# Optimization experiments

Hardware: AMD Instinct MI355X
Metric: run time of the kernel (lower is better)

The kernel has to match this reference:

```python
import jax, jax.numpy as jnp
import numpy as np
from jax import lax

LRELU = 0.1
SQRT_HALF = 0.7071067811865476
DIM = 128
NUM_PRE = 5          # dilated convs in UpsampleNet
NUM_BLOCKS = 3       # WaveNet blocks
LAYERS_PER_BLOCK = 10
NUM_WN = NUM_BLOCKS * LAYERS_PER_BLOCK  # 30


def conv1d(x, w, b, dilation=1):
    # x: [N,C,L], w: [O,I,K], 'same' padding for odd K
    k = w.shape[-1]
    pad = dilation * (k // 2)
    y = lax.conv_general_dilated(
        x, w, window_strides=(1,), padding=[(pad, pad)],
        rhs_dilation=(dilation,), dimension_numbers=('NCW', 'OIW', 'NCW'))
    return y + b[None, :, None]


def conv_transpose1d(x, w, b, stride=4):
    # kernel 4, stride 4, no padding -> L_out = 4*L
    y = lax.conv_transpose(
        x, w, strides=(stride,), padding='VALID',
        dimension_numbers=('NCW', 'OIW', 'NCW'))
    return y + b[None, :, None]


def setup_inputs() -> dict:
    key = jax.random.key(0)
    ks = iter(jax.random.split(key, 32))
    s = 0.02
    d = {}
    d['mel'] = jax.random.normal(next(ks), (4, 80, 64), jnp.float32)
    d['in_w'] = s * jax.random.normal(next(ks), (DIM, 80, 1), jnp.float32)
    d['in_b'] = jnp.zeros((DIM,), jnp.float32)
    d['pre_ws'] = s * jax.random.normal(next(ks), (NUM_PRE, DIM, DIM, 3), jnp.float32)
    d['pre_bs'] = jnp.zeros((NUM_PRE, DIM), jnp.float32)
    d['up1_w'] = s * jax.random.normal(next(ks), (DIM, DIM, 4), jnp.float32)
    d['up1_b'] = jnp.zeros((DIM,), jnp.float32)
    d['up2_w'] = s * jax.random.normal(next(ks), (DIM, DIM, 4), jnp.float32)
    d['up2_b'] = jnp.zeros((DIM,), jnp.float32)
    d['wn_ws'] = s * jax.random.normal(next(ks), (NUM_WN, 2 * DIM, DIM, 3), jnp.float32)
    d['wn_bs'] = jnp.zeros((NUM_WN, 2 * DIM), jnp.float32)
    d['sk_ws'] = s * jax.random.normal(next(ks), (NUM_WN, DIM, DIM, 1), jnp.float32)
    d['sk_bs'] = jnp.zeros((NUM_WN, DIM), jnp.float32)
    d['out1_w'] = s * jax.random.normal(next(ks), (DIM, DIM, 1), jnp.float32)
    d['out1_b'] = jnp.zeros((DIM,), jnp.float32)
    d['out2_w'] = s * jax.random.normal(next(ks), (DIM, DIM, 1), jnp.float32)
    d['out2_b'] = jnp.zeros((DIM,), jnp.float32)
    d['out3_w'] = s * jax.random.normal(next(ks), (1, DIM, 1), jnp.float32)
    d['out3_b'] = jnp.zeros((1,), jnp.float32)
    return d


def reference(mel, in_w, in_b, pre_ws, pre_bs, up1_w, up1_b, up2_w, up2_b,
              wn_ws, wn_bs, sk_ws, sk_bs,
              out1_w, out1_b, out2_w, out2_b, out3_w, out3_b):
    # ---- UpsampleNet ----
    x = conv1d(mel, in_w, in_b)                       # [N,128,T]
    for i in range(NUM_PRE):
        residual = x
        x = conv1d(x, pre_ws[i], pre_bs[i], dilation=2 ** i)
        x = jax.nn.leaky_relu(x, LRELU)
        x = (x + residual) * SQRT_HALF
    x = jax.nn.leaky_relu(conv_transpose1d(x, up1_w, up1_b), LRELU)
    x = jax.nn.leaky_relu(conv_transpose1d(x, up2_w, up2_b), LRELU)
    N, D, L = x.shape
    x = jnp.broadcast_to(x[:, :, :, None], (N, D, L, 16)).reshape(N, D, L * 16)

    # ---- WaveNet blocks (3 blocks x 10 layers) ----
    skips = jnp.zeros_like(x)
    for li in range(NUM_WN):
        dilation = 2 ** (li % LAYERS_PER_BLOCK)
        residual = x
        g = conv1d(x, wn_ws[li], wn_bs[li], dilation=dilation)  # [N,256,L]
        g_tanh, g_sig = jnp.split(g, 2, axis=1)
        gated = jnp.tanh(g_tanh) * jax.nn.sigmoid(g_sig)
        s = conv1d(gated, sk_ws[li], sk_bs[li])
        skips = skips + s
        x = s + residual

    # ---- Output stack ----
    y = jax.nn.relu(skips)
    y = jax.nn.relu(conv1d(y, out1_w, out1_b))
    y = jax.nn.relu(conv1d(y, out2_w, out2_b))
    y = conv1d(y, out3_w, out3_b)
    return jnp.tanh(y)  # [N,1,L*256]
```

## Files before the change

### kernel.cpp

```cpp
#include <hip/hip_runtime.h>
#include <math.h>

#define LRELU 0.1f
#define SQRT_HALF 0.7071067811865476f

constexpr int T_LEN = 16384;

typedef __attribute__((ext_vector_type(8))) short short8;
typedef __attribute__((ext_vector_type(4))) float f32x4;

union U4S8 { uint4 v; short8 s8; unsigned short us[8]; };

__device__ inline void bsplit(float v, unsigned short& hi, unsigned short& lo) {
    unsigned u = __float_as_uint(v);
    unsigned rh = (u + 0x7FFFu + ((u >> 16) & 1u)) >> 16;
    float fh = __uint_as_float(rh << 16);
    float r = v - fh;
    unsigned u2 = __float_as_uint(r);
    unsigned rl = (u2 + 0x7FFFu + ((u2 >> 16) & 1u)) >> 16;
    hi = (unsigned short)rh; lo = (unsigned short)rl;
}
__device__ inline float b2f(unsigned short s) { return __uint_as_float(((unsigned)s) << 16); }

__device__ inline size_t fidx(int n, int tb, int c, int l) {
    return ((size_t)((n << 10) + tb) * 4 + c) * 64 + l;
}

__device__ inline float fast_gate(float g1, float g2) {
    float ax = fabsf(g1);
    float e = __expf(ax + ax);
    float th = 1.f - 2.f * __builtin_amdgcn_rcpf(e + 1.f);
    th = __uint_as_float(__float_as_uint(th) | (__float_as_uint(g1) & 0x80000000u));
    float sg = __builtin_amdgcn_rcpf(1.f + __expf(-g2));
    return th * sg;
}

__global__ void prep_w3(const float* __restrict__ wn_ws, const float* __restrict__ sk_ws,
                        const float* __restrict__ o1w, const float* __restrict__ o2w,
                        unsigned short* __restrict__ Apk, unsigned short* __restrict__ Spk,
                        unsigned short* __restrict__ Opk1, unsigned short* __restrict__ Opk2)
{
    int b = blockIdx.x, tid = threadIdx.x;
    if (b < 360) {
        __shared__ float sl[256][32];
        int li = b / 12, ks = b % 12;
        int tap = ks >> 2, i0 = (ks & 3) * 32;
        for (int j = tid; j < 8192; j += 256) {
            int o = j >> 5, ii = j & 31;
            sl[o][ii] = wn_ws[((size_t)(li * 256 + o) * 128 + i0 + ii) * 3 + tap];
        }
        __syncthreads();
        size_t obase = ((size_t)(li * 12 + ks)) * 16384;
        for (int e = tid; e < 8192; e += 256) {
            int j = e & 7, l = (e >> 3) & 63, m16 = e >> 9;
            int o = m16 * 16 + (l & 15);
            int ii = 4 * (l >> 4) + (j & 3) + 16 * (j >> 2);
            unsigned short hi, lo; bsplit(sl[o][ii], hi, lo);
            Apk[obase + (size_t)m16 * 1024 + l * 8 + j] = hi;
            Apk[obase + (size_t)m16 * 1024 + 512 + l * 8 + j] = lo;
        }
    } else {
        __shared__ float s2[128][32];
        int bb = b - 360;
        const float* src; unsigned short* dst; int ks2;
        if (bb < 120) { int li = bb / 4; ks2 = bb % 4; src = sk_ws + (size_t)li * 16384; dst = Spk + ((size_t)(li * 4 + ks2)) * 8192; }
        else if (bb < 124) { ks2 = bb - 120; src = o1w; dst = Opk1 + (size_t)ks2 * 8192; }
        else { ks2 = bb - 124; src = o2w; dst = Opk2 + (size_t)ks2 * 8192; }
        int i0 = ks2 * 32;
        for (int j = tid; j < 4096; j += 256) {
            int o = j >> 5, ii = j & 31;
            s2[o][ii] = src[(size_t)o * 128 + i0 + ii];
        }
        __syncthreads();
        for (int e = tid; e < 4096; e += 256) {
            int j = e & 7, l = (e >> 3) & 63, m8 = e >> 9;
            int o = m8 * 16 + (l & 15);
            int ii = 4 * (l >> 4) + (j & 3) + 16 * (j >> 2);
            unsigned short hi, lo; bsplit(s2[o][ii], hi, lo);
            dst[(size_t)m8 * 1024 + l * 8 + j] = hi;
            dst[(size_t)m8 * 1024 + 512 + l * 8 + j] = lo;
        }
    }
}

__global__ void fe_in(const float* __restrict__ mel, const float* __restrict__ w,
                      const float* __restrict__ b, float* __restrict__ out)
{
    __shared__ float mc[80];
    int t = blockIdx.x, n = blockIdx.y, o = threadIdx.x;
    if (o < 80) mc[o] = mel[(n * 80 + o) * 64 + t];
    __syncthreads();
    float acc = b[o];
    #pragma unroll 8
    for (int i = 0; i < 80; i++) acc = fmaf(w[o * 80 + i], mc[i], acc);
    out[((size_t)n * 128 + o) * 64 + t] = acc;
}

__global__ void fe_pre(const float* __restrict__ in, float* __restrict__ out,
                       const float* __restrict__ w, const float* __restrict__ b, int d)
{
    __shared__ float col[3][128];
    int t = blockIdx.x, n = blockIdx.y, o = threadIdx.x;
    #pragma unroll
    for (int s = 0; s < 3; s++) {
        int tt = t + (s - 1) * d;
        col[s][o] = ((unsigned)tt < 64u) ? in[(n * 128 + o) * 64 + tt] : 0.f;
    }
    __syncthreads();
    float acc = b[o];
    const float* wo = w + o * 384;
    #pragma unroll 4
    for (int i = 0; i < 128; i++) {
        acc = fmaf(wo[i * 3 + 0], col[0][i], acc);
        acc = fmaf(wo[i * 3 + 1], col[1][i], acc);
        acc = fmaf(wo[i * 3 + 2], col[2][i], acc);
    }
    float y = acc > 0.f ? acc : LRELU * acc;
    out[(n * 128 + o) * 64 + t] = (y + in[(n * 128 + o) * 64 + t]) * SQRT_HALF;
}

__global__ __launch_bounds__(256, 4)
void fe_up3(const float* __restrict__ in, float* __restrict__ out,
            const float* __restrict__ w, const float* __restrict__ bias, int Lin)
{
    __shared__ float xs[128][16];
    const int n = blockIdx.y, qb = blockIdx.x * 16;
    const int tid = threadIdx.x;
    for (int j = tid; j < 2048; j += 256) {
        int i = j >> 4, qq = j & 15;
        xs[i][qq] = in[(size_t)(n * 128 + i) * Lin + qb + qq];
    }
    __syncthreads();
    const int o = tid & 127, qh = tid >> 7;
    float acc[8][4];
    #pragma unroll
    for (int q = 0; q < 8; q++)
        #pragma unroll
        for (int r = 0; r < 4; r++) acc[q][r] = 0.f;
    const float4* wo = (const float4*)(w + (size_t)o * 512);
    for (int i = 0; i < 128; i++) {
        float4 w4 = wo[i];
        #pragma unroll
        for (int q = 0; q < 8; q++) {
            float xv = xs[i][qh * 8 + q];
            acc[q][0] = fmaf(w4.w, xv, acc[q][0]);
            acc[q][1] = fmaf(w4.z, xv, acc[q][1]);
            acc[q][2] = fmaf(w4.y, xv, acc[q][2]);
            acc[q][3] = fmaf(w4.x, xv, acc[q][3]);
        }
    }
    float bo = bias[o];
    const int Lout = 4 * Lin;
    #pragma unroll
    for (int q = 0; q < 8; q++) {
        float4 v;
        float a0 = acc[q][0] + bo, a1 = acc[q][1] + bo, a2 = acc[q][2] + bo, a3 = acc[q][3] + bo;
        v.x = a0 > 0.f ? a0 : LRELU * a0;
        v.y = a1 > 0.f ? a1 : LRELU * a1;
        v.z = a2 > 0.f ? a2 : LRELU * a2;
        v.w = a3 > 0.f ? a3 : LRELU * a3;
        *(float4*)(out + (size_t)(n * 128 + o) * Lout + (size_t)(qb + qh * 8 + q) * 4) = v;
    }
}

__global__ void fe_repeat_f(const float* __restrict__ x1024,
                            uint4* __restrict__ Xh, uint4* __restrict__ Xl)
{
    __shared__ float sx[128][65];
    const int n = blockIdx.y, tbq = blockIdx.x;
    const int tid = threadIdx.x;
    for (int j = tid; j < 8192; j += 256) {
        int ch = j >> 6, col = j & 63;
        sx[ch][col] = x1024[(size_t)(n * 128 + ch) * 1024 + tbq * 64 + col];
    }
    __syncthreads();
    for (int m = tid; m < 16384; m += 256) {
        int l = m & 63, c = (m >> 6) & 3, tbr = m >> 8;
        U4S8 ho, lo_;
        #pragma unroll
        for (int j = 0; j < 8; j++) {
            int ch = 32 * c + 4 * (l >> 4) + (j & 3) + 16 * (j >> 2);
            unsigned short hi, lo; bsplit(sx[ch][tbr], hi, lo);
            ho.us[j] = hi; lo_.us[j] = lo;
        }
        size_t gi = fidx(n, tbq * 64 + tbr, c, l);
        Xh[gi] = ho.v; Xl[gi] = lo_.v;
    }
}

__global__ __launch_bounds__(256, 4)
void wn_layer(const uint4* __restrict__ Xh, const uint4* __restrict__ Xl,
              uint4* __restrict__ Yh, uint4* __restrict__ Yl,
              const unsigned short* __restrict__ Apk, const float* __restrict__ gb,
              const unsigned short* __restrict__ Spk, const float* __restrict__ skb, int dil)
{
    __shared__ __align__(16) uint4 S[2048];

    const int bxs = ((blockIdx.x & 7) << 5) | (blockIdx.x >> 3);
    const int n = blockIdx.y, tb0 = bxs * 4, t0 = tb0 * 16;
    const int tid = threadIdx.x, lane = tid & 63, wid = tid >> 6;

    f32x4 acc[4][4];
    const f32x4 z4 = {0.f, 0.f, 0.f, 0.f};
    #pragma unroll
    for (int mf = 0; mf < 4; mf++)
        #pragma unroll
        for (int nf = 0; nf < 4; nf++) acc[mf][nf] = z4;

    const short8* ap = (const short8*)Apk;
    const int m16c[4] = {2 * wid, 2 * wid + 1, 8 + 2 * wid, 9 + 2 * wid};

    for (int s = 0; s < 3; s++) {
        const int sh = (s - 1) * dil;
        __syncthreads();
        for (int j = tid; j < 1024; j += 256) {
            int l = j & 63, c = (j >> 6) & 3, nf = j >> 8;
            int t = t0 + nf * 16 + (l & 15) + sh;
            uint4 vh = make_uint4(0u, 0u, 0u, 0u), vl = vh;
            if ((unsigned)t < (unsigned)T_LEN) {
                size_t gi = fidx(n, t >> 4, c, (l & 48) | (t & 15));
                vh = Xh[gi]; vl = Xl[gi];
            }
            S[j] = vh; S[1024 + j] = vl;
        }
        __syncthreads();
        for (int c = 0; c < 4; c++) {
            const int ks = s * 4 + c;
            short8 Ah[4], Al[4];
            #pragma unroll
            for (int mf = 0; mf < 4; mf++) {
                int ib = (ks * 16 + m16c[mf]) * 128 + lane;
                Ah[mf] = ap[ib];
                Al[mf] = ap[ib + 64];
            }
            #pragma unroll
            for (int nf = 0; nf < 4; nf++) {
                U4S8 bh, bl;
                bh.v = S[(nf * 4 + c) * 64 + lane];
                bl.v = S[1024 + (nf * 4 + c) * 64 + lane];
                #pragma unroll
                for (int mf = 0; mf < 4; mf++) {
                    acc[mf][nf] = __builtin_amdgcn_mfma_f32_16x16x32_bf16(Ah[mf], bh.s8, acc[mf][nf], 0, 0, 0);
                    acc[mf][nf] = __builtin_amdgcn_mfma_f32_16x16x32_bf16(Al[mf], bh.s8, acc[mf][nf], 0, 0, 0);
                    acc[mf][nf] = __builtin_amdgcn_mfma_f32_16x16x32_bf16(Ah[mf], bl.s8, acc[mf][nf], 0, 0, 0);
                }
            }
        }
    }
    __syncthreads();

    const int cb = 4 * (lane >> 4);
    float bt[2][4], bsg[2][4];
    #pragma unroll
    for (int mf2 = 0; mf2 < 2; mf2++)
        #pragma unroll
        for (int r = 0; r < 4; r++) {
            int ch = (2 * wid + mf2) * 16 + cb + r;
            bt[mf2][r] = gb[ch];
            bsg[mf2][r] = gb[128 + ch];
        }
    #pragma unroll
    for (int nf = 0; nf < 4; nf++) {
        U4S8 h4, l4;
        #pragma unroll
        for (int mf2 = 0; mf2 < 2; mf2++)
            #pragma unroll
            for (int r = 0; r < 4; r++) {
                float g1 = acc[mf2][nf][r] + bt[mf2][r];
                float g2 = acc[mf2 + 2][nf][r] + bsg[mf2][r];
                float gv = fast_gate(g1, g2);
                unsigned short hi, lo; bsplit(gv, hi, lo);
                h4.us[mf2 * 4 + r] = hi;
                l4.us[mf2 * 4 + r] = lo;
            }
        S[(nf * 4 + wid) * 64 + lane] = h4.v;
        S[1024 + (nf * 4 + wid) * 64 + lane] = l4.v;
    }
    __syncthreads();

    f32x4 acc2[2][4];
    #pragma unroll
    for (int mf2 = 0; mf2 < 2; mf2++)
        #pragma unroll
        for (int nf = 0; nf < 4; nf++) acc2[mf2][nf] = z4;
    const short8* sp = (const short8*)Spk;
    #pragma unroll
    for (int c = 0; c < 4; c++) {
        short8 A2h[2], A2l[2];
        #pragma unroll
        for (int mf2 = 0; mf2 < 2; mf2++) {
            int ib = (c * 8 + 2 * wid + mf2) * 128 + lane;
            A2h[mf2] = sp[ib];
            A2l[mf2] = sp[ib + 64];
        }
        #pragma unroll
        for (int nf = 0; nf < 4; nf++) {
            U4S8 bh, bl;
            bh.v = S[(nf * 4 + c) * 64 + lane];
            bl.v = S[1024 + (nf * 4 + c) * 64 + lane];
            #pragma unroll
            for (int mf2 = 0; mf2 < 2; mf2++) {
                acc2[mf2][nf] = __builtin_amdgcn_mfma_f32_16x16x32_bf16(A2h[mf2], bh.s8, acc2[mf2][nf], 0, 0, 0);
                acc2[mf2][nf] = __builtin_amdgcn_mfma_f32_16x16x32_bf16(A2l[mf2], bh.s8, acc2[mf2][nf], 0, 0, 0);
                acc2[mf2][nf] = __builtin_amdgcn_mfma_f32_16x16x32_bf16(A2h[mf2], bl.s8, acc2[mf2][nf], 0, 0, 0);
            }
        }
    }

    float bo2[2][4];
    #pragma unroll
    for (int mf2 = 0; mf2 < 2; mf2++)
        #pragma unroll
        for (int r = 0; r < 4; r++) bo2[mf2][r] = skb[(2 * wid + mf2) * 16 + cb + r];
    #pragma unroll
    for (int nf = 0; nf < 4; nf++) {
        size_t gi = fidx(n, tb0 + nf, wid, lane);
        U4S8 xh, xl, oh, ol;
        xh.v = Xh[gi]; xl.v = Xl[gi];
        #pragma unroll
        for (int j = 0; j < 8; j++) {
            int mf2 = j >> 2, r = j & 3;
            float xin = b2f(xh.us[j]) + b2f(xl.us[j]);
            float sv = acc2[mf2][nf][r] + bo2[mf2][r];
            unsigned short hi, lo; bsplit(sv + xin, hi, lo);
            oh.us[j] = hi; ol.us[j] = lo;
        }
        Yh[gi] = oh.v; Yl[gi] = ol.v;
    }
}

__global__ __launch_bounds__(256, 2)
void os_fused(const uint4* __restrict__ Fh, const uint4* __restrict__ Fl,
              const uint4* __restrict__ Ih, const uint4* __restrict__ Il,
              const unsigned short* __restrict__ Opk1, const float* __restrict__ o1b,
              const unsigned short* __restrict__ Opk2, const float* __restrict__ o2b,
              const float* __restrict__ o3w, const float* __restrict__ o3b,
              float* __restrict__ out)
{
    __shared__ __align__(16) uint4 SA[2048];
    __shared__ __align__(16) uint4 SB[2048];
    const int n = blockIdx.y, tb0 = blockIdx.x * 4, t0 = tb0 * 16;
    const int tid = threadIdx.x, lane = tid & 63, wid = tid >> 6;
    const int tl = lane & 15, cb = 4 * (lane >> 4);
    const f32x4 z4 = {0.f, 0.f, 0.f, 0.f};
    char* ldsA = (char*)SA;

    for (int j = tid; j < 1024; j += 256) {
        int l = j & 63, c = (j >> 6) & 3, nf = j >> 8;
        size_t gi = fidx(n, tb0 + nf, c, l);
        U4S8 fh, fl, ih, il, ho, lo_;
        fh.v = Fh[gi]; fl.v = Fl[gi]; ih.v = Ih[gi]; il.v = Il[gi];
        #pragma unroll
        for (int e = 0; e < 8; e++) {
            float d = (b2f(fh.us[e]) + b2f(fl.us[e])) - (b2f(ih.us[e]) + b2f(il.us[e]));
            d = fmaxf(d, 0.f);
            unsigned short hi, lo; bsplit(d, hi, lo);
            ho.us[e] = hi; lo_.us[e] = lo;
        }
        SA[j] = ho.v; SA[1024 + j] = lo_.v;
    }
    __syncthreads();

    {
        f32x4 acc[2][4];
        #pragma unroll
        for (int mf2 = 0; mf2 < 2; mf2++)
            #pragma unroll
            for (int nf = 0; nf < 4; nf++) acc[mf2][nf] = z4;
        const short8* op = (const short8*)Opk1;
        #pragma unroll
        for (int c = 0; c < 4; c++) {
            short8 Ah[2], Al[2];
            #pragma unroll
            for (int mf2 = 0; mf2 < 2; mf2++) {
                int ib = (c * 8 + 2 * wid + mf2) * 128 + lane;
                Ah[mf2] = op[ib]; Al[mf2] = op[ib + 64];
            }
            #pragma unroll
            for (int nf = 0; nf < 4; nf++) {
                U4S8 bh, bl;
                bh.v = SA[(nf * 4 + c) * 64 + lane];
                bl.v = SA[1024 + (nf * 4 + c) * 64 + lane];
                #pragma unroll
                for (int mf2 = 0; mf2 < 2; mf2++) {
                    acc[mf2][nf] = __builtin_amdgcn_mfma_f32_16x16x32_bf16(Ah[mf2], bh.s8, acc[mf2][nf], 0, 0, 0);
                    acc[mf2][nf] = __builtin_amdgcn_mfma_f32_16x16x32_bf16(Al[mf2], bh.s8, acc[mf2][nf], 0, 0, 0);
                    acc[mf2][nf] = __builtin_amdgcn_mfma_f32_16x16x32_bf16(Ah[mf2], bl.s8, acc[mf2][nf], 0, 0, 0);
                }
            }
        }
        #pragma unroll
        for (int nf = 0; nf < 4; nf++) {
            U4S8 h4, l4;
            #pragma unroll
            for (int mf2 = 0; mf2 < 2; mf2++)
                #pragma unroll
                for (int r = 0; r < 4; r++) {
                    float v = fmaxf(acc[mf2][nf][r] + o1b[(2 * wid + mf2) * 16 + cb + r], 0.f);
                    unsigned short hi, lo; bsplit(v, hi, lo);
                    h4.us[mf2 * 4 + r] = hi; l4.us[mf2 * 4 + r] = lo;
                }
            SB[(nf * 4 + wid) * 64 + lane] = h4.v;
            SB[1024 + (nf * 4 + wid) * 64 + lane] = l4.v;
        }
    }
    __syncthreads();

    {
        f32x4 acc[2][4];
        #pragma unroll
        for (int mf2 = 0; mf2 < 2; mf2++)
            #pragma unroll
            for (int nf = 0; nf < 4; nf++) acc[mf2][nf] = z4;
        const short8* op = (const short8*)Opk2;
        #pragma unroll
        for (int c = 0; c < 4; c++) {
            short8 Ah[2], Al[2];
            #pragma unroll
            for (int mf2 = 0; mf2 < 2; mf2++) {
                int ib = (c * 8 + 2 * wid + mf2) * 128 + lane;
                Ah[mf2] = op[ib]; Al[mf2] = op[ib + 64];
            }
            #pragma unroll
            for (int nf = 0; nf < 4; nf++) {
                U4S8 bh, bl;
                bh.v = SB[(nf * 4 + c) * 64 + lane];
                bl.v = SB[1024 + (nf * 4 + c) * 64 + lane];
                #pragma unroll
                for (int mf2 = 0; mf2 < 2; mf2++) {
                    acc[mf2][nf] = __builtin_amdgcn_mfma_f32_16x16x32_bf16(Ah[mf2], bh.s8, acc[mf2][nf], 0, 0, 0);
                    acc[mf2][nf] = __builtin_amdgcn_mfma_f32_16x16x32_bf16(Al[mf2], bh.s8, acc[mf2][nf], 0, 0, 0);
                    acc[mf2][nf] = __builtin_amdgcn_mfma_f32_16x16x32_bf16(Ah[mf2], bl.s8, acc[mf2][nf], 0, 0, 0);
                }
            }
        }
        __syncthreads();
        #pragma unroll
        for (int mf2 = 0; mf2 < 2; mf2++) {
            const int ch0 = (2 * wid + mf2) * 16 + cb;
            #pragma unroll
            for (int nf = 0; nf < 4; nf++) {
                int row = nf * 16 + tl, swz = (row & 7) << 4;
                float4 v;
                v.x = fmaxf(acc[mf2][nf][0] + o2b[ch0 + 0], 0.f);
                v.y = fmaxf(acc[mf2][nf][1] + o2b[ch0 + 1], 0.f);
                v.z = fmaxf(acc[mf2][nf][2] + o2b[ch0 + 2], 0.f);
                v.w = fmaxf(acc[mf2][nf][3] + o2b[ch0 + 3], 0.f);
                *(float4*)(ldsA + row * 512 + ((ch0 * 4) ^ swz)) = v;
            }
        }
    }
    __syncthreads();

    {
        const int t_loc = tid >> 2, qq = tid & 3;
        const int row = t_loc, swz = (row & 7) << 4;
        float a = 0.f;
        #pragma unroll
        for (int cc = 0; cc < 8; cc++) {
            int ch = qq * 32 + cc * 4;
            float4 v = *(const float4*)(ldsA + row * 512 + ((ch * 4) ^ swz));
            a += o3w[ch] * v.x + o3w[ch + 1] * v.y + o3w[ch + 2] * v.z + o3w[ch + 3] * v.w;
        }
        a += __shfl_xor(a, 1);
        a += __shfl_xor(a, 2);
        if (qq == 0) out[(size_t)n * T_LEN + t0 + t_loc] = tanhf(a + o3b[0]);
    }
}

extern "C" void kernel_launch(void* const* d_in, const int* in_sizes, int n_in,
                              void* d_out, int out_size, void* d_ws, size_t ws_size,
                              hipStream_t stream)
{
    (void)in_sizes; (void)n_in; (void)out_size; (void)ws_size;
    const float* mel    = (const float*)d_in[0];
    const float* in_w   = (const float*)d_in[1];
    const float* in_b   = (const float*)d_in[2];
    const float* pre_w  = (const float*)d_in[3];
    const float* pre_b  = (const float*)d_in[4];
    const float* up1_w  = (const float*)d_in[5];
    const float* up1_b  = (const float*)d_in[6];
    const float* up2_w  = (const float*)d_in[7];
    const float* up2_b  = (const float*)d_in[8];
    const float* wn_wsp = (const float*)d_in[9];
    const float* wn_bs  = (const float*)d_in[10];
    const float* sk_wsp = (const float*)d_in[11];
    const float* sk_bs  = (const float*)d_in[12];
    const float* o1w = (const float*)d_in[13];
    const float* o1b = (const float*)d_in[14];
    const float* o2w = (const float*)d_in[15];
    const float* o2b = (const float*)d_in[16];
    const float* o3w = (const float*)d_in[17];
    const float* o3b = (const float*)d_in[18];

    char* base = (char*)d_ws;
    uint4* XAh = (uint4*)(base);
    uint4* XAl = (uint4*)(base + 16777216);
    uint4* XBh = (uint4*)(base + 33554432);
    uint4* XBl = (uint4*)(base + 50331648);
    uint4* XCh = (uint4*)(base + 67108864);
    uint4* XCl = (uint4*)(base + 83886080);
    unsigned short* Apk = (unsigned short*)(base + 100663296);
    unsigned short* Spk = (unsigned short*)(base + 112459776);
    unsigned short* Opk1 = (unsigned short*)(base + 114425856);
    unsigned short* Opk2 = (unsigned short*)(base + 114491392);
    float* a64   = (float*)(base + 114556928);
    float* b64   = (float*)(base + 114688000);
    float* x256  = (float*)(base + 114819072);
    float* x1024 = (float*)(base + 115343360);

    prep_w3<<<488, 256, 0, stream>>>(wn_wsp, sk_wsp, o1w, o2w, Apk, Spk, Opk1, Opk2);

    fe_in<<<dim3(64, 4), 128, 0, stream>>>(mel, in_w, in_b, a64);
    fe_pre<<<dim3(64, 4), 128, 0, stream>>>(a64, b64, pre_w + 0 * 49152, pre_b + 0 * 128, 1);
    fe_pre<<<dim3(64, 4), 128, 0, stream>>>(b64, a64, pre_w + 1 * 49152, pre_b + 1 * 128, 2);
    fe_pre<<<dim3(64, 4), 128, 0, stream>>>(a64, b64, pre_w + 2 * 49152, pre_b + 2 * 128, 4);
    fe_pre<<<dim3(64, 4), 128, 0, stream>>>(b64, a64, pre_w + 3 * 49152, pre_b + 3 * 128, 8);
    fe_pre<<<dim3(64, 4), 128, 0, stream>>>(a64, b64, pre_w + 4 * 49152, pre_b + 4 * 128, 16);
    fe_up3<<<dim3(4, 4), 256, 0, stream>>>(b64, x256, up1_w, up1_b, 64);
    fe_up3<<<dim3(16, 4), 256, 0, stream>>>(x256, x1024, up2_w, up2_b, 256);
    fe_repeat_f<<<dim3(16, 4), 256, 0, stream>>>(x1024, XAh, XAl);

    for (int li = 0; li < 30; li++) {
        int d = 1 << (li % 10);
        const uint4 *ih, *il; uint4 *oh, *ol;
        if (li == 0)      { ih = XAh; il = XAl; oh = XBh; ol = XBl; }
        else if (li & 1)  { ih = XBh; il = XBl; oh = XCh; ol = XCl; }
        else              { ih = XCh; il = XCl; oh = XBh; ol = XBl; }
        wn_layer<<<dim3(T_LEN / 64, 4), 256, 0, stream>>>(
            ih, il, oh, ol,
            Apk + (size_t)li * 196608, wn_bs + li * 256,
            Spk + (size_t)li * 32768, sk_bs + li * 128, d);
    }

    os_fused<<<dim3(T_LEN / 64, 4), 256, 0, stream>>>(
        XCh, XCl, XAh, XAl, Opk1, o1b, Opk2, o2b, o3w, o3b, (float*)d_out);
}
```

Measured before the change: 1.887 ms.

## Add direct-global-load WaveNet layer variant for tile-aligned dilations

For dilations that are multiples of 16, the shifted input tiles line up with whole time blocks, so a new kernel variant feeds the MFMAs straight from global memory and skips the shared-memory staging and its barriers. Smaller dilations keep the staged path, which now has its inner channel loop fully unrolled. The shared gate/skip tail is factored into a helper, and the block-index swizzle is removed from both variants. Loading directly from global removes the three staging barriers per layer, but relies on the L2 cache to serve the reuse across warps and may change locality now that the swizzle is gone.

```diff
diff --git a/kernel.cpp b/kernel.cpp
--- a/kernel.cpp
+++ b/kernel.cpp
@@ -188,16 +188,155 @@
     }
 }
 
+__device__ __forceinline__ void wn_tail(
+    f32x4 (&acc)[4][4], uint4* S, const uint4* __restrict__ Xh, const uint4* __restrict__ Xl,
+    uint4* __restrict__ Yh, uint4* __restrict__ Yl,
+    const float* __restrict__ gb, const unsigned short* __restrict__ Spk,
+    const float* __restrict__ skb, int n, int tb0, int lane, int wid)
+{
+    const f32x4 z4 = {0.f, 0.f, 0.f, 0.f};
+    const int cb = 4 * (lane >> 4);
+    float bt[2][4], bsg[2][4];
+    #pragma unroll
+    for (int mf2 = 0; mf2 < 2; mf2++)
+        #pragma unroll
+        for (int r = 0; r < 4; r++) {
+            int ch = (2 * wid + mf2) * 16 + cb + r;
+            bt[mf2][r] = gb[ch];
+            bsg[mf2][r] = gb[128 + ch];
+        }
+    #pragma unroll
+    for (int nf = 0; nf < 4; nf++) {
+        U4S8 h4, l4;
+        #pragma unroll
+        for (int mf2 = 0; mf2 < 2; mf2++)
+            #pragma unroll
+            for (int r = 0; r < 4; r++) {
+                float g1 = acc[mf2][nf][r] + bt[mf2][r];
+                float g2 = acc[mf2 + 2][nf][r] + bsg[mf2][r];
+                float gv = fast_gate(g1, g2);
+                unsigned short hi, lo; bsplit(gv, hi, lo);
+                h4.us[mf2 * 4 + r] = hi;
+                l4.us[mf2 * 4 + r] = lo;
+            }
+        S[(nf * 4 + wid) * 64 + lane] = h4.v;
+        S[1024 + (nf * 4 + wid) * 64 + lane] = l4.v;
+    }
+    __syncthreads();
+
+    f32x4 acc2[2][4];
+    #pragma unroll
+    for (int mf2 = 0; mf2 < 2; mf2++)
+        #pragma unroll
+        for (int nf = 0; nf < 4; nf++) acc2[mf2][nf] = z4;
+    const short8* sp = (const short8*)Spk;
+    #pragma unroll
+    for (int c = 0; c < 4; c++) {
+        short8 A2h[2], A2l[2];
+        #pragma unroll
+        for (int mf2 = 0; mf2 < 2; mf2++) {
+            int ib = (c * 8 + 2 * wid + mf2) * 128 + lane;
+            A2h[mf2] = sp[ib];
+            A2l[mf2] = sp[ib + 64];
+        }
+        #pragma unroll
+        for (int nf = 0; nf < 4; nf++) {
+            U4S8 bh, bl;
+            bh.v = S[(nf * 4 + c) * 64 + lane];
+            bl.v = S[1024 + (nf * 4 + c) * 64 + lane];
+            #pragma unroll
+            for (int mf2 = 0; mf2 < 2; mf2++) {
+                acc2[mf2][nf] = __builtin_amdgcn_mfma_f32_16x16x32_bf16(A2h[mf2], bh.s8, acc2[mf2][nf], 0, 0, 0);
+                acc2[mf2][nf] = __builtin_amdgcn_mfma_f32_16x16x32_bf16(A2l[mf2], bh.s8, acc2[mf2][nf], 0, 0, 0);
+                acc2[mf2][nf] = __builtin_amdgcn_mfma_f32_16x16x32_bf16(A2h[mf2], bl.s8, acc2[mf2][nf], 0, 0, 0);
+            }
+        }
+    }
+
+    float bo2[2][4];
+    #pragma unroll
+    for (int mf2 = 0; mf2 < 2; mf2++)
+        #pragma unroll
+        for (int r = 0; r < 4; r++) bo2[mf2][r] = skb[(2 * wid + mf2) * 16 + cb + r];
+    #pragma unroll
+    for (int nf = 0; nf < 4; nf++) {
+        size_t gi = fidx(n, tb0 + nf, wid, lane);
+        U4S8 xh, xl, oh, ol;
+        xh.v = Xh[gi]; xl.v = Xl[gi];
+        #pragma unroll
+        for (int j = 0; j < 8; j++) {
+            int mf2 = j >> 2, r = j & 3;
+            float xin = b2f(xh.us[j]) + b2f(xl.us[j]);
+            float sv = acc2[mf2][nf][r] + bo2[mf2][r];
+            unsigned short hi, lo; bsplit(sv + xin, hi, lo);
+            oh.us[j] = hi; ol.us[j] = lo;
+        }
+        Yh[gi] = oh.v; Yl[gi] = ol.v;
+    }
+}
+
 __global__ __launch_bounds__(256, 4)
-void wn_layer(const uint4* __restrict__ Xh, const uint4* __restrict__ Xl,
-              uint4* __restrict__ Yh, uint4* __restrict__ Yl,
-              const unsigned short* __restrict__ Apk, const float* __restrict__ gb,
-              const unsigned short* __restrict__ Spk, const float* __restrict__ skb, int dil)
+void wn_layer_d(const uint4* __restrict__ Xh, const uint4* __restrict__ Xl,
+                uint4* __restrict__ Yh, uint4* __restrict__ Yl,
+                const unsigned short* __restrict__ Apk, const float* __restrict__ gb,
+                const unsigned short* __restrict__ Spk, const float* __restrict__ skb, int dq)
 {
     __shared__ __align__(16) uint4 S[2048];
-
-    const int bxs = ((blockIdx.x & 7) << 5) | (blockIdx.x >> 3);
-    const int n = blockIdx.y, tb0 = bxs * 4, t0 = tb0 * 16;
+    const int n = blockIdx.y, tb0 = blockIdx.x * 4;
+    const int tid = threadIdx.x, lane = tid & 63, wid = tid >> 6;
+
+    f32x4 acc[4][4];
+    const f32x4 z4 = {0.f, 0.f, 0.f, 0.f};
+    #pragma unroll
+    for (int mf = 0; mf < 4; mf++)
+        #pragma unroll
+        for (int nf = 0; nf < 4; nf++) acc[mf][nf] = z4;
+
+    const short8* ap = (const short8*)Apk;
+    const int m16c[4] = {2 * wid, 2 * wid + 1, 8 + 2 * wid, 9 + 2 * wid};
+
+    #pragma unroll
+    for (int s = 0; s < 3; s++) {
+        const int tbS = tb0 + (s - 1) * dq;
+        #pragma unroll
+        for (int c = 0; c < 4; c++) {
+            const int ks = s * 4 + c;
+            short8 Ah[4], Al[4];
+            #pragma unroll
+            for (int mf = 0; mf < 4; mf++) {
+                int ib = (ks * 16 + m16c[mf]) * 128 + lane;
+                Ah[mf] = ap[ib];
+                Al[mf] = ap[ib + 64];
+            }
+            #pragma unroll
+            for (int nf = 0; nf < 4; nf++) {
+                int tb = tbS + nf;
+                bool ok = ((unsigned)tb < 1024u);
+                int tbc = ok ? tb : 0;
+                size_t gi = fidx(n, tbc, c, lane);
+                U4S8 bh, bl;
+                bh.v = Xh[gi]; bl.v = Xl[gi];
+                if (!ok) { bh.v = make_uint4(0u,0u,0u,0u); bl.v = make_uint4(0u,0u,0u,0u); }
+                #pragma unroll
+                for (int mf = 0; mf < 4; mf++) {
+                    acc[mf][nf] = __builtin_amdgcn_mfma_f32_16x16x32_bf16(Ah[mf], bh.s8, acc[mf][nf], 0, 0, 0);
+                    acc[mf][nf] = __builtin_amdgcn_mfma_f32_16x16x32_bf16(Al[mf], bh.s8, acc[mf][nf], 0, 0, 0);
+                    acc[mf][nf] = __builtin_amdgcn_mfma_f32_16x16x32_bf16(Ah[mf], bl.s8, acc[mf][nf], 0, 0, 0);
+                }
+            }
+        }
+    }
+    wn_tail(acc, S, Xh, Xl, Yh, Yl, gb, Spk, skb, n, tb0, lane, wid);
+}
+
+__global__ __launch_bounds__(256, 4)
+void wn_layer_s(const uint4* __restrict__ Xh, const uint4* __restrict__ Xl,
+                uint4* __restrict__ Yh, uint4* __restrict__ Yl,
+                const unsigned short* __restrict__ Apk, const float* __restrict__ gb,
+                const unsigned short* __restrict__ Spk, const float* __restrict__ skb, int dil)
+{
+    __shared__ __align__(16) uint4 S[2048];
+    const int n = blockIdx.y, tb0 = blockIdx.x * 4, t0 = tb0 * 16;
     const int tid = threadIdx.x, lane = tid & 63, wid = tid >> 6;
 
     f32x4 acc[4][4];
@@ -224,6 +363,7 @@
             S[j] = vh; S[1024 + j] = vl;
         }
         __syncthreads();
+        #pragma unroll
         for (int c = 0; c < 4; c++) {
             const int ks = s * 4 + c;
             short8 Ah[4], Al[4];
@@ -248,85 +388,7 @@
         }
     }
     __syncthreads();
-
-    const int cb = 4 * (lane >> 4);
-    float bt[2][4], bsg[2][4];
-    #pragma unroll
-    for (int mf2 = 0; mf2 < 2; mf2++)
-        #pragma unroll
-        for (int r = 0; r < 4; r++) {
-            int ch = (2 * wid + mf2) * 16 + cb + r;
-            bt[mf2][r] = gb[ch];
-            bsg[mf2][r] = gb[128 + ch];
-        }
-    #pragma unroll
-    for (int nf = 0; nf < 4; nf++) {
-        U4S8 h4, l4;
-        #pragma unroll
-        for (int mf2 = 0; mf2 < 2; mf2++)
-            #pragma unroll
-            for (int r = 0; r < 4; r++) {
-                float g1 = acc[mf2][nf][r] + bt[mf2][r];
-                float g2 = acc[mf2 + 2][nf][r] + bsg[mf2][r];
-                float gv = fast_gate(g1, g2);
-                unsigned short hi, lo; bsplit(gv, hi, lo);
-                h4.us[mf2 * 4 + r] = hi;
-                l4.us[mf2 * 4 + r] = lo;
-            }
-        S[(nf * 4 + wid) * 64 + lane] = h4.v;
-        S[1024 + (nf * 4 + wid) * 64 + lane] = l4.v;
-    }
-    __syncthreads();
-
-    f32x4 acc2[2][4];
-    #pragma unroll
-    for (int mf2 = 0; mf2 < 2; mf2++)
-        #pragma unroll
-        for (int nf = 0; nf < 4; nf++) acc2[mf2][nf] = z4;
-    const short8* sp = (const short8*)Spk;
-    #pragma unroll
-    for (int c = 0; c < 4; c++) {
-        short8 A2h[2], A2l[2];
-        #pragma unroll
-        for (int mf2 = 0; mf2 < 2; mf2++) {
-            int ib = (c * 8 + 2 * wid + mf2) * 128 + lane;
-            A2h[mf2] = sp[ib];
-            A2l[mf2] = sp[ib + 64];
-        }
-        #pragma unroll
-        for (int nf = 0; nf < 4; nf++) {
-            U4S8 bh, bl;
-            bh.v = S[(nf * 4 + c) * 64 + lane];
-            bl.v = S[1024 + (nf * 4 + c) * 64 + lane];
-            #pragma unroll
-            for (int mf2 = 0; mf2 < 2; mf2++) {
-                acc2[mf2][nf] = __builtin_amdgcn_mfma_f32_16x16x32_bf16(A2h[mf2], bh.s8, acc2[mf2][nf], 0, 0, 0);
-                acc2[mf2][nf] = __builtin_amdgcn_mfma_f32_16x16x32_bf16(A2l[mf2], bh.s8, acc2[mf2][nf], 0, 0, 0);
-                acc2[mf2][nf] = __builtin_amdgcn_mfma_f32_16x16x32_bf16(A2h[mf2], bl.s8, acc2[mf2][nf], 0, 0, 0);
-            }
-        }
-    }
-
-    float bo2[2][4];
-    #pragma unroll
-    for (int mf2 = 0; mf2 < 2; mf2++)
-        #pragma unroll
-        for (int r = 0; r < 4; r++) bo2[mf2][r] = skb[(2 * wid + mf2) * 16 + cb + r];
-    #pragma unroll
-    for (int nf = 0; nf < 4; nf++) {
-        size_t gi = fidx(n, tb0 + nf, wid, lane);
-        U4S8 xh, xl, oh, ol;
-        xh.v = Xh[gi]; xl.v = Xl[gi];
-        #pragma unroll
-        for (int j = 0; j < 8; j++) {
-            int mf2 = j >> 2, r = j & 3;
-            float xin = b2f(xh.us[j]) + b2f(xl.us[j]);
-            float sv = acc2[mf2][nf][r] + bo2[mf2][r];
-            unsigned short hi, lo; bsplit(sv + xin, hi, lo);
-            oh.us[j] = hi; ol.us[j] = lo;
-        }
-        Yh[gi] = oh.v; Yl[gi] = ol.v;
-    }
+    wn_tail(acc, S, Xh, Xl, Yh, Yl, gb, Spk, skb, n, tb0, lane, wid);
 }
 
 __global__ __launch_bounds__(256, 2)
@@ -527,10 +589,17 @@
         if (li == 0)      { ih = XAh; il = XAl; oh = XBh; ol = XBl; }
         else if (li & 1)  { ih = XBh; il = XBl; oh = XCh; ol = XCl; }
         else              { ih = XCh; il = XCl; oh = XBh; ol = XBl; }
-        wn_layer<<<dim3(T_LEN / 64, 4), 256, 0, stream>>>(
-            ih, il, oh, ol,
-            Apk + (size_t)li * 196608, wn_bs + li * 256,
-            Spk + (size_t)li * 32768, sk_bs + li * 128, d);
+        if (d >= 16) {
+            wn_layer_d<<<dim3(T_LEN / 64, 4), 256, 0, stream>>>(
+                ih, il, oh, ol,
+                Apk + (size_t)li * 196608, wn_bs + li * 256,
+                Spk + (size_t)li * 32768, sk_bs + li * 128, d >> 4);
+        } else {
+            wn_layer_s<<<dim3(T_LEN / 64, 4), 256, 0, stream>>>(
+                ih, il, oh, ol,
+                Apk + (size_t)li * 196608, wn_bs + li * 256,
+                Spk + (size_t)li * 32768, sk_bs + li * 128, d);
+        }
     }
 
     os_fused<<<dim3(T_LEN / 64, 4), 256, 0, stream>>>(
```

New measurement: 2.121 ms. +12.4%, slower.
